# Optimization experiments

Hardware: AMD Instinct MI355X
Metric: run time of the kernel (lower is better)

## Reference

```python
import jax, jax.numpy as jnp
import numpy as np

STATE_DIM = 256
MAX_NODES = 64
EPS = 1e-5
EDGE_THRESHOLD = 0.3


def _glorot(key, shape):
    fan_in = shape[0]
    bound = 1.0 / np.sqrt(fan_in)
    return jax.random.uniform(key, shape, jnp.float32, -bound, bound)


def setup_inputs() -> dict:
    key = jax.random.key(0)
    ks = jax.random.split(key, 16)
    D = STATE_DIM
    d2, d4 = D // 2, D // 4
    inp = {
        "state_sequence": jax.random.normal(ks[0], (256, 128, D), jnp.float32),
        # node encoder
        "W1": _glorot(ks[1], (D, d2)), "b1": jnp.zeros((d2,), jnp.float32),
        "W2": _glorot(ks[2], (d2, d4)), "b2": jnp.zeros((d4,), jnp.float32),
        "gamma": jnp.ones((d4,), jnp.float32), "beta": jnp.zeros((d4,), jnp.float32),
        # edge predictor (input dim d2 = 2*d4)
        "E1": _glorot(ks[3], (d2, 64)), "bE1": jnp.zeros((64,), jnp.float32),
        "E2": _glorot(ks[4], (64, 32)), "bE2": jnp.zeros((32,), jnp.float32),
        "E3": _glorot(ks[5], (32, 1)), "bE3": jnp.zeros((1,), jnp.float32),
        # strength estimator
        "S1": _glorot(ks[6], (d2, 32)), "bS1": jnp.zeros((32,), jnp.float32),
        "S2": _glorot(ks[7], (32, 1)), "bS2": jnp.zeros((1,), jnp.float32),
    }
    return inp


def reference(state_sequence, W1, b1, W2, b2, gamma, beta,
              E1, bE1, E2, bE2, E3, bE3, S1, bS1, S2, bS2):
    B, S, D = state_sequence.shape
    N = MAX_NODES
    # pad if seq shorter than max_nodes (static shapes, here S >= N so no-op branch)
    if S < N:
        state_sequence = jnp.pad(state_sequence, ((0, 0), (0, N - S), (0, 0)))
        S = N
    # linspace indices, truncated to long like torch.linspace(..., dtype=long)
    idx = jnp.linspace(0.0, S - 1, N).astype(jnp.int32)
    nodes = state_sequence[:, idx]                      # [B, N, D]

    # node encoder: Linear -> ReLU -> (Dropout eval) -> Linear -> LayerNorm
    h = jax.nn.relu(jnp.einsum('bnd,de->bne', nodes, W1) + b1)
    h = jnp.einsum('bnd,de->bne', h, W2) + b2           # [B, N, D//4]
    mu = jnp.mean(h, axis=-1, keepdims=True)
    var = jnp.mean((h - mu) ** 2, axis=-1, keepdims=True)
    node_features = (h - mu) * jax.lax.rsqrt(var + EPS) * gamma + beta
    node_features = jnp.nan_to_num(node_features, nan=0.0)

    d4 = node_features.shape[-1]
    # pair input is concat([f_i, f_j]); split first-layer weights to avoid
    # materializing the [B,N,N,2*d4] concat tensor.
    # edge predictor first layer
    ei = jnp.einsum('bnd,dh->bnh', node_features, E1[:d4])   # [B, N, 64]
    ej = jnp.einsum('bnd,dh->bnh', node_features, E1[d4:])
    he = jax.nn.relu(ei[:, :, None, :] + ej[:, None, :, :] + bE1)  # [B,N,N,64]
    he = jax.nn.relu(jnp.einsum('bijh,hk->bijk', he, E2) + bE2)    # [B,N,N,32]
    edge_prob = jax.nn.sigmoid(jnp.einsum('bijk,ko->bijo', he, E3) + bE3)[..., 0]

    # strength estimator
    si = jnp.einsum('bnd,dh->bnh', node_features, S1[:d4])
    sj = jnp.einsum('bnd,dh->bnh', node_features, S1[d4:])
    hs = jax.nn.relu(si[:, :, None, :] + sj[:, None, :, :] + bS1)  # [B,N,N,32]
    strength = jnp.tanh(jnp.einsum('bijk,ko->bijo', hs, S2) + bS2)[..., 0]

    offdiag = 1.0 - jnp.eye(N, dtype=edge_prob.dtype)   # i != j only
    adjacency = edge_prob * offdiag
    strengths = strength * offdiag
    adjacency = jnp.where(adjacency > EDGE_THRESHOLD, adjacency, 0.0)
    return node_features, adjacency, strengths
```

## Files before the change

### kernel.cpp

```cpp
#include <hip/hip_runtime.h>
#include <hip/hip_bf16.h>
#include <math.h>

typedef __attribute__((ext_vector_type(8))) short short8;
typedef __attribute__((ext_vector_type(4))) short short4v;
typedef __attribute__((ext_vector_type(4))) float f32x4;
typedef __attribute__((ext_vector_type(2))) _Float16 h2;
typedef __attribute__((ext_vector_type(4))) _Float16 h4;
typedef __attribute__((ext_vector_type(8))) _Float16 h8;

__device__ __forceinline__ short f2bf(float f) {
    __hip_bfloat16 h = __float2bfloat16(f);
    return __builtin_bit_cast(short, h);
}

__global__ __launch_bounds__(256)
void kernelA0(const float* __restrict__ W1, const float* __restrict__ W2,
              const float* __restrict__ E1, const float* __restrict__ S1,
              short* __restrict__ wT)
{
    const int tid = blockIdx.x * 256 + threadIdx.x;
    {
        const int k = tid >> 7, n = tid & 127;
        wT[n * 256 + k] = f2bf(W1[tid]);
    }
    if (tid < 8192) {
        const int k = tid >> 6, n = tid & 63;
        wT[32768 + n * 128 + k] = f2bf(W2[tid]);
    }
    if (tid < 8192) {
        const int rr = tid >> 6, c = tid & 63;
        const int o = (rr < 64) ? c : (64 + c);
        const int k = (rr < 64) ? rr : (rr - 64);
        wT[40960 + o * 64 + k] = f2bf(E1[tid]);
    }
    if (tid < 4096) {
        const int rr = tid >> 5, c = tid & 31;
        const int o = (rr < 64) ? (128 + c) : (160 + c);
        const int k = (rr < 64) ? rr : (rr - 64);
        wT[40960 + o * 64 + k] = f2bf(S1[tid]);
    }
}

constexpr int XS_S  = 264;
constexpr int H1B_S = 136;
constexpr int HS_S  = 68;
constexpr int NNF_S = 72;
constexpr int EJW   = 72;
constexpr int SJW   = 40;

constexpr int OFF_XS  = 0;
constexpr int OFF_EIH = 0;
constexpr int OFF_EJH = 9216;
constexpr int OFF_SIH = 18432;
constexpr int OFF_SJH = 23552;
constexpr int OFF_H1B = 33792;
constexpr int OFF_HS  = 51200;
constexpr int LDS_BYTES = 68608;

__global__ __launch_bounds__(1024)
void kernelF(const float* __restrict__ x,
             const float* __restrict__ b1, const float* __restrict__ b2,
             const float* __restrict__ gamma, const float* __restrict__ beta,
             const short* __restrict__ wT,
             const float* __restrict__ bE1, const float* __restrict__ E2,
             const float* __restrict__ bE2, const float* __restrict__ E3,
             const float* __restrict__ bE3, const float* __restrict__ bS1,
             const float* __restrict__ S2, const float* __restrict__ bS2,
             float* __restrict__ out_nf, float* __restrict__ out_adj,
             float* __restrict__ out_str)
{
    extern __shared__ char lds[];
    short*    XsS  = (short*)(lds + OFF_XS);
    short*    h1BS = (short*)(lds + OFF_H1B);
    float*    HsS  = (float*)(lds + OFF_HS);
    short*    nfBS = (short*)(lds + OFF_H1B);
    _Float16* eihS = (_Float16*)(lds + OFF_EIH);
    _Float16* ejhS = (_Float16*)(lds + OFF_EJH);
    _Float16* sihS = (_Float16*)(lds + OFF_SIH);
    _Float16* sjhS = (_Float16*)(lds + OFF_SJH);
    __shared__ float bE2s[32], E3s[32];
    __shared__ _Float16 s2hS[32];

    const int t = threadIdx.x, b = blockIdx.x;
    const int w = t >> 6, l = t & 63, g = l >> 4, r = l & 15;
    const short* W1T = wT;
    const short* W2T = wT + 32768;
    const short* WcT = wT + 40960;

    if (t < 32)       bE2s[t] = bE2[t];
    else if (t < 64)  E3s[t - 32] = E3[t - 32];
    else if (t < 96)  s2hS[t - 64] = (_Float16)S2[t - 64];

    h8 aE00, aE10, aE01, aE11;
#pragma unroll
    for (int e = 0; e < 8; ++e) {
        aE00[e] = (_Float16)E2[(size_t)(8 * g + e) * 32 + r];
        aE10[e] = (_Float16)E2[(size_t)(8 * g + e + 32) * 32 + r];
        aE01[e] = (_Float16)E2[(size_t)(8 * g + e) * 32 + r + 16];
        aE11[e] = (_Float16)E2[(size_t)(8 * g + e + 32) * 32 + r + 16];
    }
    const float bE3v = bE3[0], bS2v = bS2[0];
    const h8 z8 = {(_Float16)0.f, (_Float16)0.f, (_Float16)0.f, (_Float16)0.f,
                   (_Float16)0.f, (_Float16)0.f, (_Float16)0.f, (_Float16)0.f};

    {
        const int row = t >> 4, c0 = t & 15;
        const int srow = (row == 63) ? 127 : (int)((float)row * (127.0f / 63.0f));
        const float* xrow = x + ((size_t)b * 128 + srow) * 256;
#pragma unroll
        for (int i = 0; i < 4; ++i) {
            const int c4 = (c0 + 16 * i) * 4;
            const float4 v = *(const float4*)(xrow + c4);
            short4v s;
            s[0] = f2bf(v.x); s[1] = f2bf(v.y); s[2] = f2bf(v.z); s[3] = f2bf(v.w);
            *(short4v*)&XsS[row * XS_S + c4] = s;
        }
    }
    __syncthreads();

    {
        const int mt = w >> 2, nb = (w & 3) << 1;
        const int aRow = (16 * mt + r) * XS_S;
#pragma unroll
        for (int np = 0; np < 2; ++np) {
            const int n = ((nb + np) << 4) + r;
            f32x4 acca = {0.f, 0.f, 0.f, 0.f};
            f32x4 accb = {0.f, 0.f, 0.f, 0.f};
#pragma unroll
            for (int ks = 0; ks < 4; ++ks) {
                const short8 a0  = *(const short8*)&XsS[aRow + 32 * ks + 8 * g];
                const short8 a1  = *(const short8*)&XsS[aRow + 32 * (ks + 4) + 8 * g];
                const short8 bwa = *(const short8*)(W1T + (size_t)n * 256 + 32 * ks + 8 * g);
                const short8 bwb = *(const short8*)(W1T + (size_t)n * 256 + 32 * (ks + 4) + 8 * g);
                acca = __builtin_amdgcn_mfma_f32_16x16x32_bf16(a0, bwa, acca, 0, 0, 0);
                accb = __builtin_amdgcn_mfma_f32_16x16x32_bf16(a1, bwb, accb, 0, 0, 0);
            }
            const float b1v = b1[n];
#pragma unroll
            for (int q = 0; q < 4; ++q)
                h1BS[(16 * mt + 4 * g + q) * H1B_S + n] = f2bf(fmaxf(acca[q] + accb[q] + b1v, 0.f));
        }
    }
    __syncthreads();

    {
        const int mt = w >> 2;
        const int n = ((w & 3) << 4) + r;
        const int aRow = (16 * mt + r) * H1B_S;
        f32x4 acca = {0.f, 0.f, 0.f, 0.f};
        f32x4 accb = {0.f, 0.f, 0.f, 0.f};
#pragma unroll
        for (int ks2 = 0; ks2 < 2; ++ks2) {
            const short8 ha0 = *(const short8*)&h1BS[aRow + 32 * (2 * ks2) + 8 * g];
            const short8 ha1 = *(const short8*)&h1BS[aRow + 32 * (2 * ks2 + 1) + 8 * g];
            const short8 bw0 = *(const short8*)(W2T + (size_t)n * 128 + 32 * (2 * ks2) + 8 * g);
            const short8 bw1 = *(const short8*)(W2T + (size_t)n * 128 + 32 * (2 * ks2 + 1) + 8 * g);
            acca = __builtin_amdgcn_mfma_f32_16x16x32_bf16(ha0, bw0, acca, 0, 0, 0);
            accb = __builtin_amdgcn_mfma_f32_16x16x32_bf16(ha1, bw1, accb, 0, 0, 0);
        }
        const float b2v = b2[n];
#pragma unroll
        for (int q = 0; q < 4; ++q)
            HsS[(16 * mt + 4 * g + q) * HS_S + n] = acca[q] + accb[q] + b2v;
    }
    __syncthreads();

    {
        const int row = t >> 4, c4 = (t & 15) * 4;
        const float4 v = *(const float4*)&HsS[row * HS_S + c4];
        float s = v.x + v.y + v.z + v.w;
        s += __shfl_xor(s, 1); s += __shfl_xor(s, 2);
        s += __shfl_xor(s, 4); s += __shfl_xor(s, 8);
        const float mu = s * (1.0f / 64.0f);
        float vs = 0.f;
        { const float d0 = v.x-mu, d1 = v.y-mu, d2 = v.z-mu, d3 = v.w-mu;
          vs = fmaf(d0,d0, fmaf(d1,d1, fmaf(d2,d2, d3*d3))); }
        vs += __shfl_xor(vs, 1); vs += __shfl_xor(vs, 2);
        vs += __shfl_xor(vs, 4); vs += __shfl_xor(vs, 8);
        const float rstd = rsqrtf(vs * (1.0f / 64.0f) + 1e-5f);
        const float4 gv = *(const float4*)(gamma + c4);
        const float4 bv = *(const float4*)(beta  + c4);
        float4 o;
        o.x = fmaf((v.x - mu) * rstd, gv.x, bv.x);
        o.y = fmaf((v.y - mu) * rstd, gv.y, bv.y);
        o.z = fmaf((v.z - mu) * rstd, gv.z, bv.z);
        o.w = fmaf((v.w - mu) * rstd, gv.w, bv.w);
        *(float4*)(out_nf + (size_t)b * 4096 + (size_t)row * 64 + c4) = o;
        short4v ob;
        ob[0] = f2bf(o.x); ob[1] = f2bf(o.y); ob[2] = f2bf(o.z); ob[3] = f2bf(o.w);
        *(short4v*)&nfBS[row * NNF_S + c4] = ob;
    }
    __syncthreads();

    {
        const int mt = w >> 2;
        const short8 na0 = *(const short8*)&nfBS[(16 * mt + r) * NNF_S + 8 * g];
        const short8 na1 = *(const short8*)&nfBS[(16 * mt + r) * NNF_S + 32 + 8 * g];
#pragma unroll
        for (int k3 = 0; k3 < 3; ++k3) {
            const int ot = (w & 3) * 3 + k3;
            const int c = 16 * ot + r;
            const short8 bw0 = *(const short8*)(WcT + (size_t)c * 64 + 8 * g);
            const short8 bw1 = *(const short8*)(WcT + (size_t)c * 64 + 32 + 8 * g);
            f32x4 acc = {0.f, 0.f, 0.f, 0.f};
            acc = __builtin_amdgcn_mfma_f32_16x16x32_bf16(na0, bw0, acc, 0, 0, 0);
            acc = __builtin_amdgcn_mfma_f32_16x16x32_bf16(na1, bw1, acc, 0, 0, 0);
            if (ot < 4) {
                const float bv = bE1[c];
#pragma unroll
                for (int q = 0; q < 4; ++q)
                    eihS[(16 * mt + 4 * g + q) * EJW + c] = (_Float16)(acc[q] + bv);
            } else if (ot < 8) {
#pragma unroll
                for (int q = 0; q < 4; ++q)
                    ejhS[(16 * mt + 4 * g + q) * EJW + (c - 64)] = (_Float16)acc[q];
            } else if (ot < 10) {
                const float bv = bS1[c - 128];
#pragma unroll
                for (int q = 0; q < 4; ++q)
                    sihS[(16 * mt + 4 * g + q) * SJW + (c - 128)] = (_Float16)(acc[q] + bv);
            } else {
#pragma unroll
                for (int q = 0; q < 4; ++q)
                    sjhS[(16 * mt + 4 * g + q) * SJW + (c - 160)] = (_Float16)acc[q];
            }
        }
    }
    __syncthreads();

    for (int jt = 0; jt < 4; ++jt) {
        const int j = (jt << 4) + r;
        const h8 ej0 = *(const h8*)&ejhS[j * EJW + 8 * g];
        const h8 ej1 = *(const h8*)&ejhS[j * EJW + 32 + 8 * g];

#pragma unroll
        for (int ii = 0; ii < 4; ++ii) {
            const int ig = 4 * w + ii;
            const h8 ei0 = *(const h8*)&eihS[ig * EJW + 8 * g];
            const h8 ei1 = *(const h8*)&eihS[ig * EJW + 32 + 8 * g];

            const h8 b0 = __builtin_elementwise_max(ei0 + ej0, z8);
            const h8 b1 = __builtin_elementwise_max(ei1 + ej1, z8);

            f32x4 acc0 = {0.f, 0.f, 0.f, 0.f};
            f32x4 acc1 = {0.f, 0.f, 0.f, 0.f};
            acc0 = __builtin_amdgcn_mfma_f32_16x16x32_f16(aE00, b0, acc0, 0, 0, 0);
            acc0 = __builtin_amdgcn_mfma_f32_16x16x32_f16(aE10, b1, acc0, 0, 0, 0);
            acc1 = __builtin_amdgcn_mfma_f32_16x16x32_f16(aE01, b0, acc1, 0, 0, 0);
            acc1 = __builtin_amdgcn_mfma_f32_16x16x32_f16(aE11, b1, acc1, 0, 0, 0);

            float pe = 0.f;
#pragma unroll
            for (int q = 0; q < 4; ++q) {
                const int k0 = 4 * g + q;
                pe = fmaf(fmaxf(acc0[q] + bE2s[k0], 0.f), E3s[k0], pe);
                pe = fmaf(fmaxf(acc1[q] + bE2s[k0 + 16], 0.f), E3s[k0 + 16], pe);
            }
            pe += __shfl_xor(pe, 16);
            pe += __shfl_xor(pe, 32);

            if (l < 16) {
                const float z = pe + bE3v;
                const float p = 1.0f / (1.0f + __expf(-z));
                const float av = (j == ig || !(p > 0.3f)) ? 0.f : p;
                out_adj[(size_t)b * 4096 + (size_t)ig * 64 + j] = av;
            }
        }
    }

    {
        const int j = t & 63;
        const int ib = (t >> 6) * 4;
#pragma unroll
        for (int ii = 0; ii < 4; ++ii) {
            const int ig = ib + ii;
            float sacc = 0.f;
#pragma unroll
            for (int c = 0; c < 4; ++c) {
                const h8 si8 = *(const h8*)&sihS[ig * SJW + 8 * c];
                const h8 sj8 = *(const h8*)&sjhS[j * SJW + 8 * c];
                const h8 s2  = *(const h8*)&s2hS[8 * c];
                const h8 hs = __builtin_elementwise_max(si8 + sj8, z8);
                const h2 p0 = __builtin_shufflevector(hs, hs, 0, 1);
                const h2 p1 = __builtin_shufflevector(hs, hs, 2, 3);
                const h2 p2 = __builtin_shufflevector(hs, hs, 4, 5);
                const h2 p3 = __builtin_shufflevector(hs, hs, 6, 7);
                const h2 q0 = __builtin_shufflevector(s2, s2, 0, 1);
                const h2 q1 = __builtin_shufflevector(s2, s2, 2, 3);
                const h2 q2 = __builtin_shufflevector(s2, s2, 4, 5);
                const h2 q3 = __builtin_shufflevector(s2, s2, 6, 7);
                sacc = __builtin_amdgcn_fdot2(p0, q0, sacc, false);
                sacc = __builtin_amdgcn_fdot2(p1, q1, sacc, false);
                sacc = __builtin_amdgcn_fdot2(p2, q2, sacc, false);
                sacc = __builtin_amdgcn_fdot2(p3, q3, sacc, false);
            }
            const float xs = sacc + bS2v;
            const float e2x = __expf(2.0f * xs);
            const float sv = (j == ig) ? 0.f : (e2x - 1.0f) / (e2x + 1.0f);
            out_str[(size_t)b * 4096 + (size_t)ig * 64 + j] = sv;
        }
    }
}

extern "C" void kernel_launch(void* const* d_in, const int* in_sizes, int n_in,
                              void* d_out, int out_size, void* d_ws, size_t ws_size,
                              hipStream_t stream)
{
    const float* x     = (const float*)d_in[0];
    const float* W1    = (const float*)d_in[1];
    const float* b1    = (const float*)d_in[2];
    const float* W2    = (const float*)d_in[3];
    const float* b2    = (const float*)d_in[4];
    const float* gamma = (const float*)d_in[5];
    const float* beta  = (const float*)d_in[6];
    const float* E1    = (const float*)d_in[7];
    const float* bE1   = (const float*)d_in[8];
    const float* E2    = (const float*)d_in[9];
    const float* bE2   = (const float*)d_in[10];
    const float* E3    = (const float*)d_in[11];
    const float* bE3   = (const float*)d_in[12];
    const float* S1    = (const float*)d_in[13];
    const float* bS1   = (const float*)d_in[14];
    const float* S2    = (const float*)d_in[15];
    const float* bS2   = (const float*)d_in[16];

    float* out     = (float*)d_out;
    float* out_nf  = out;
    float* out_adj = out + 1048576;
    float* out_str = out + 2097152;

    short* wT = (short*)d_ws;

    (void)hipFuncSetAttribute((const void*)kernelF,
        hipFuncAttributeMaxDynamicSharedMemorySize, LDS_BYTES);

    kernelA0<<<128, 256, 0, stream>>>(W1, W2, E1, S1, wT);

    kernelF<<<256, 1024, LDS_BYTES, stream>>>(
        x, b1, b2, gamma, beta, wT,
        bE1, E2, bE2, E3, bE3, bS1, S2, bS2,
        out_nf, out_adj, out_str);
}
```

Measured before the change: 38.45 us.

## Split each batch across two 512-thread blocks, duplicating node encoder work

Launches a 2x256 grid of 512-thread blocks instead of 256 blocks of 1024 threads. Each block recomputes the full node encoder and projections for its batch element, then handles half of the i-rows of the pairwise edge and strength stages. Only block s==0 writes node features. The aim is more blocks across the CUs and better occupancy, paid for by computing the encoder and projections twice per batch element.

```diff
diff --git a/kernel.cpp b/kernel.cpp
--- a/kernel.cpp
+++ b/kernel.cpp
@@ -6,7 +6,6 @@
 typedef __attribute__((ext_vector_type(4))) short short4v;
 typedef __attribute__((ext_vector_type(4))) float f32x4;
 typedef __attribute__((ext_vector_type(2))) _Float16 h2;
-typedef __attribute__((ext_vector_type(4))) _Float16 h4;
 typedef __attribute__((ext_vector_type(8))) _Float16 h8;
 
 __device__ __forceinline__ short f2bf(float f) {
@@ -58,7 +57,7 @@
 constexpr int OFF_HS  = 51200;
 constexpr int LDS_BYTES = 68608;
 
-__global__ __launch_bounds__(1024)
+__global__ __launch_bounds__(512)
 void kernelF(const float* __restrict__ x,
              const float* __restrict__ b1, const float* __restrict__ b2,
              const float* __restrict__ gamma, const float* __restrict__ beta,
@@ -82,7 +81,9 @@
     __shared__ float bE2s[32], E3s[32];
     __shared__ _Float16 s2hS[32];
 
-    const int t = threadIdx.x, b = blockIdx.x;
+    const int t = threadIdx.x;
+    const int s = blockIdx.x;
+    const int b = blockIdx.y;
     const int w = t >> 6, l = t & 63, g = l >> 4, r = l & 15;
     const short* W1T = wT;
     const short* W2T = wT + 32768;
@@ -105,25 +106,25 @@
                    (_Float16)0.f, (_Float16)0.f, (_Float16)0.f, (_Float16)0.f};
 
     {
-        const int row = t >> 4, c0 = t & 15;
+        const int row = t >> 3, c0 = t & 7;
         const int srow = (row == 63) ? 127 : (int)((float)row * (127.0f / 63.0f));
         const float* xrow = x + ((size_t)b * 128 + srow) * 256;
 #pragma unroll
-        for (int i = 0; i < 4; ++i) {
-            const int c4 = (c0 + 16 * i) * 4;
+        for (int i = 0; i < 8; ++i) {
+            const int c4 = (c0 + 8 * i) * 4;
             const float4 v = *(const float4*)(xrow + c4);
-            short4v s;
-            s[0] = f2bf(v.x); s[1] = f2bf(v.y); s[2] = f2bf(v.z); s[3] = f2bf(v.w);
-            *(short4v*)&XsS[row * XS_S + c4] = s;
-        }
-    }
-    __syncthreads();
-
-    {
-        const int mt = w >> 2, nb = (w & 3) << 1;
+            short4v sv4;
+            sv4[0] = f2bf(v.x); sv4[1] = f2bf(v.y); sv4[2] = f2bf(v.z); sv4[3] = f2bf(v.w);
+            *(short4v*)&XsS[row * XS_S + c4] = sv4;
+        }
+    }
+    __syncthreads();
+
+    {
+        const int mt = w >> 1, nb = (w & 1) << 2;
         const int aRow = (16 * mt + r) * XS_S;
 #pragma unroll
-        for (int np = 0; np < 2; ++np) {
+        for (int np = 0; np < 4; ++np) {
             const int n = ((nb + np) << 4) + r;
             f32x4 acca = {0.f, 0.f, 0.f, 0.f};
             f32x4 accb = {0.f, 0.f, 0.f, 0.f};
@@ -145,34 +146,38 @@
     __syncthreads();
 
     {
-        const int mt = w >> 2;
-        const int n = ((w & 3) << 4) + r;
+        const int mt = w >> 1;
         const int aRow = (16 * mt + r) * H1B_S;
-        f32x4 acca = {0.f, 0.f, 0.f, 0.f};
-        f32x4 accb = {0.f, 0.f, 0.f, 0.f};
-#pragma unroll
-        for (int ks2 = 0; ks2 < 2; ++ks2) {
-            const short8 ha0 = *(const short8*)&h1BS[aRow + 32 * (2 * ks2) + 8 * g];
-            const short8 ha1 = *(const short8*)&h1BS[aRow + 32 * (2 * ks2 + 1) + 8 * g];
-            const short8 bw0 = *(const short8*)(W2T + (size_t)n * 128 + 32 * (2 * ks2) + 8 * g);
-            const short8 bw1 = *(const short8*)(W2T + (size_t)n * 128 + 32 * (2 * ks2 + 1) + 8 * g);
-            acca = __builtin_amdgcn_mfma_f32_16x16x32_bf16(ha0, bw0, acca, 0, 0, 0);
-            accb = __builtin_amdgcn_mfma_f32_16x16x32_bf16(ha1, bw1, accb, 0, 0, 0);
-        }
-        const float b2v = b2[n];
-#pragma unroll
-        for (int q = 0; q < 4; ++q)
-            HsS[(16 * mt + 4 * g + q) * HS_S + n] = acca[q] + accb[q] + b2v;
-    }
-    __syncthreads();
-
-    {
-        const int row = t >> 4, c4 = (t & 15) * 4;
+#pragma unroll
+        for (int p = 0; p < 2; ++p) {
+            const int n = (((w & 1) * 2 + p) << 4) + r;
+            f32x4 acca = {0.f, 0.f, 0.f, 0.f};
+            f32x4 accb = {0.f, 0.f, 0.f, 0.f};
+#pragma unroll
+            for (int ks2 = 0; ks2 < 2; ++ks2) {
+                const short8 ha0 = *(const short8*)&h1BS[aRow + 32 * (2 * ks2) + 8 * g];
+                const short8 ha1 = *(const short8*)&h1BS[aRow + 32 * (2 * ks2 + 1) + 8 * g];
+                const short8 bw0 = *(const short8*)(W2T + (size_t)n * 128 + 32 * (2 * ks2) + 8 * g);
+                const short8 bw1 = *(const short8*)(W2T + (size_t)n * 128 + 32 * (2 * ks2 + 1) + 8 * g);
+                acca = __builtin_amdgcn_mfma_f32_16x16x32_bf16(ha0, bw0, acca, 0, 0, 0);
+                accb = __builtin_amdgcn_mfma_f32_16x16x32_bf16(ha1, bw1, accb, 0, 0, 0);
+            }
+            const float b2v = b2[n];
+#pragma unroll
+            for (int q = 0; q < 4; ++q)
+                HsS[(16 * mt + 4 * g + q) * HS_S + n] = acca[q] + accb[q] + b2v;
+        }
+    }
+    __syncthreads();
+
+#pragma unroll
+    for (int it = 0; it < 2; ++it) {
+        const int row = (t >> 4) + 32 * it, c4 = (t & 15) * 4;
         const float4 v = *(const float4*)&HsS[row * HS_S + c4];
-        float s = v.x + v.y + v.z + v.w;
-        s += __shfl_xor(s, 1); s += __shfl_xor(s, 2);
-        s += __shfl_xor(s, 4); s += __shfl_xor(s, 8);
-        const float mu = s * (1.0f / 64.0f);
+        float sm = v.x + v.y + v.z + v.w;
+        sm += __shfl_xor(sm, 1); sm += __shfl_xor(sm, 2);
+        sm += __shfl_xor(sm, 4); sm += __shfl_xor(sm, 8);
+        const float mu = sm * (1.0f / 64.0f);
         float vs = 0.f;
         { const float d0 = v.x-mu, d1 = v.y-mu, d2 = v.z-mu, d3 = v.w-mu;
           vs = fmaf(d0,d0, fmaf(d1,d1, fmaf(d2,d2, d3*d3))); }
@@ -186,7 +191,8 @@
         o.y = fmaf((v.y - mu) * rstd, gv.y, bv.y);
         o.z = fmaf((v.z - mu) * rstd, gv.z, bv.z);
         o.w = fmaf((v.w - mu) * rstd, gv.w, bv.w);
-        *(float4*)(out_nf + (size_t)b * 4096 + (size_t)row * 64 + c4) = o;
+        if (s == 0)
+            *(float4*)(out_nf + (size_t)b * 4096 + (size_t)row * 64 + c4) = o;
         short4v ob;
         ob[0] = f2bf(o.x); ob[1] = f2bf(o.y); ob[2] = f2bf(o.z); ob[3] = f2bf(o.w);
         *(short4v*)&nfBS[row * NNF_S + c4] = ob;
@@ -194,12 +200,12 @@
     __syncthreads();
 
     {
-        const int mt = w >> 2;
+        const int mt = w >> 1;
         const short8 na0 = *(const short8*)&nfBS[(16 * mt + r) * NNF_S + 8 * g];
         const short8 na1 = *(const short8*)&nfBS[(16 * mt + r) * NNF_S + 32 + 8 * g];
 #pragma unroll
-        for (int k3 = 0; k3 < 3; ++k3) {
-            const int ot = (w & 3) * 3 + k3;
+        for (int k6 = 0; k6 < 6; ++k6) {
+            const int ot = (w & 1) * 6 + k6;
             const int c = 16 * ot + r;
             const short8 bw0 = *(const short8*)(WcT + (size_t)c * 64 + 8 * g);
             const short8 bw1 = *(const short8*)(WcT + (size_t)c * 64 + 32 + 8 * g);
@@ -236,7 +242,7 @@
 
 #pragma unroll
         for (int ii = 0; ii < 4; ++ii) {
-            const int ig = 4 * w + ii;
+            const int ig = 32 * s + 4 * w + ii;
             const h8 ei0 = *(const h8*)&eihS[ig * EJW + 8 * g];
             const h8 ei1 = *(const h8*)&eihS[ig * EJW + 32 + 8 * g];
 
@@ -271,7 +277,7 @@
 
     {
         const int j = t & 63;
-        const int ib = (t >> 6) * 4;
+        const int ib = 32 * s + (t >> 6) * 4;
 #pragma unroll
         for (int ii = 0; ii < 4; ++ii) {
             const int ig = ib + ii;
@@ -337,7 +343,7 @@
 
     kernelA0<<<128, 256, 0, stream>>>(W1, W2, E1, S1, wT);
 
-    kernelF<<<256, 1024, LDS_BYTES, stream>>>(
+    kernelF<<<dim3(2, 256), 512, LDS_BYTES, stream>>>(
         x, b1, b2, gamma, beta, wT,
         bE1, E2, bE2, E3, bE3, bS1, S2, bS2,
         out_nf, out_adj, out_str);
```

Measured after the change: 47.74 us. 1.24x slower.

## Split fused kernel into node encoder and pairwise edge kernel with finer grid

Applied to the files above, without the earlier changes.

Splits the single per-batch fused kernel into a node-encoder kernel that writes per-node edge and strength projections to global workspace, and a separate pairwise kernel launched on an 8x256 grid of 256-thread blocks. Each pairwise block loads the j-side projections plus 8 i-rows into LDS and computes edge probabilities and strengths for that slice. This is meant to raise parallelism and occupancy in the pairwise phase, which previously ran as only 256 large blocks. In exchange it adds a kernel launch and a global round trip for the intermediate projections.

```diff
diff --git a/kernel.cpp b/kernel.cpp
--- a/kernel.cpp
+++ b/kernel.cpp
@@ -6,7 +6,6 @@
 typedef __attribute__((ext_vector_type(4))) short short4v;
 typedef __attribute__((ext_vector_type(4))) float f32x4;
 typedef __attribute__((ext_vector_type(2))) _Float16 h2;
-typedef __attribute__((ext_vector_type(4))) _Float16 h4;
 typedef __attribute__((ext_vector_type(8))) _Float16 h8;
 
 __device__ __forceinline__ short f2bf(float f) {
@@ -20,90 +19,54 @@
               short* __restrict__ wT)
 {
     const int tid = blockIdx.x * 256 + threadIdx.x;
-    {
-        const int k = tid >> 7, n = tid & 127;
-        wT[n * 256 + k] = f2bf(W1[tid]);
-    }
+    {   const int k = tid >> 7, n = tid & 127;
+        wT[n * 256 + k] = f2bf(W1[tid]); }
     if (tid < 8192) {
         const int k = tid >> 6, n = tid & 63;
-        wT[32768 + n * 128 + k] = f2bf(W2[tid]);
-    }
+        wT[32768 + n * 128 + k] = f2bf(W2[tid]); }
     if (tid < 8192) {
         const int rr = tid >> 6, c = tid & 63;
         const int o = (rr < 64) ? c : (64 + c);
         const int k = (rr < 64) ? rr : (rr - 64);
-        wT[40960 + o * 64 + k] = f2bf(E1[tid]);
-    }
+        wT[40960 + o * 64 + k] = f2bf(E1[tid]); }
     if (tid < 4096) {
         const int rr = tid >> 5, c = tid & 31;
         const int o = (rr < 64) ? (128 + c) : (160 + c);
         const int k = (rr < 64) ? rr : (rr - 64);
-        wT[40960 + o * 64 + k] = f2bf(S1[tid]);
-    }
+        wT[40960 + o * 64 + k] = f2bf(S1[tid]); }
 }
 
 constexpr int XS_S  = 264;
 constexpr int H1B_S = 136;
 constexpr int HS_S  = 68;
 constexpr int NNF_S = 72;
-constexpr int EJW   = 72;
-constexpr int SJW   = 40;
-
 constexpr int OFF_XS  = 0;
-constexpr int OFF_EIH = 0;
-constexpr int OFF_EJH = 9216;
-constexpr int OFF_SIH = 18432;
-constexpr int OFF_SJH = 23552;
 constexpr int OFF_H1B = 33792;
 constexpr int OFF_HS  = 51200;
-constexpr int LDS_BYTES = 68608;
+constexpr int LDS_BYTES_N = 68608;
 
 __global__ __launch_bounds__(1024)
-void kernelF(const float* __restrict__ x,
+void kernelN(const float* __restrict__ x,
              const float* __restrict__ b1, const float* __restrict__ b2,
              const float* __restrict__ gamma, const float* __restrict__ beta,
              const short* __restrict__ wT,
-             const float* __restrict__ bE1, const float* __restrict__ E2,
-             const float* __restrict__ bE2, const float* __restrict__ E3,
-             const float* __restrict__ bE3, const float* __restrict__ bS1,
-             const float* __restrict__ S2, const float* __restrict__ bS2,
-             float* __restrict__ out_nf, float* __restrict__ out_adj,
-             float* __restrict__ out_str)
+             const float* __restrict__ bE1, const float* __restrict__ bS1,
+             float* __restrict__ out_nf,
+             _Float16* __restrict__ wei, _Float16* __restrict__ wej,
+             _Float16* __restrict__ wsi, _Float16* __restrict__ wsj)
 {
     extern __shared__ char lds[];
-    short*    XsS  = (short*)(lds + OFF_XS);
-    short*    h1BS = (short*)(lds + OFF_H1B);
-    float*    HsS  = (float*)(lds + OFF_HS);
-    short*    nfBS = (short*)(lds + OFF_H1B);
-    _Float16* eihS = (_Float16*)(lds + OFF_EIH);
-    _Float16* ejhS = (_Float16*)(lds + OFF_EJH);
-    _Float16* sihS = (_Float16*)(lds + OFF_SIH);
-    _Float16* sjhS = (_Float16*)(lds + OFF_SJH);
-    __shared__ float bE2s[32], E3s[32];
-    __shared__ _Float16 s2hS[32];
+    short* XsS  = (short*)(lds + OFF_XS);
+    short* h1BS = (short*)(lds + OFF_H1B);
+    float* HsS  = (float*)(lds + OFF_HS);
+    short* nfBS = (short*)(lds + OFF_H1B);
 
     const int t = threadIdx.x, b = blockIdx.x;
-    const int w = t >> 6, l = t & 63, g = l >> 4, r = l & 15;
+    const int w = t >> 6, g = (t & 63) >> 4, r = t & 15;
     const short* W1T = wT;
     const short* W2T = wT + 32768;
     const short* WcT = wT + 40960;
 
-    if (t < 32)       bE2s[t] = bE2[t];
-    else if (t < 64)  E3s[t - 32] = E3[t - 32];
-    else if (t < 96)  s2hS[t - 64] = (_Float16)S2[t - 64];
-
-    h8 aE00, aE10, aE01, aE11;
-#pragma unroll
-    for (int e = 0; e < 8; ++e) {
-        aE00[e] = (_Float16)E2[(size_t)(8 * g + e) * 32 + r];
-        aE10[e] = (_Float16)E2[(size_t)(8 * g + e + 32) * 32 + r];
-        aE01[e] = (_Float16)E2[(size_t)(8 * g + e) * 32 + r + 16];
-        aE11[e] = (_Float16)E2[(size_t)(8 * g + e + 32) * 32 + r + 16];
-    }
-    const float bE3v = bE3[0], bS2v = bS2[0];
-    const h8 z8 = {(_Float16)0.f, (_Float16)0.f, (_Float16)0.f, (_Float16)0.f,
-                   (_Float16)0.f, (_Float16)0.f, (_Float16)0.f, (_Float16)0.f};
-
     {
         const int row = t >> 4, c0 = t & 15;
         const int srow = (row == 63) ? 127 : (int)((float)row * (127.0f / 63.0f));
@@ -112,9 +75,9 @@
         for (int i = 0; i < 4; ++i) {
             const int c4 = (c0 + 16 * i) * 4;
             const float4 v = *(const float4*)(xrow + c4);
-            short4v s;
-            s[0] = f2bf(v.x); s[1] = f2bf(v.y); s[2] = f2bf(v.z); s[3] = f2bf(v.w);
-            *(short4v*)&XsS[row * XS_S + c4] = s;
+            short4v sv;
+            sv[0] = f2bf(v.x); sv[1] = f2bf(v.y); sv[2] = f2bf(v.z); sv[3] = f2bf(v.w);
+            *(short4v*)&XsS[row * XS_S + c4] = sv;
         }
     }
     __syncthreads();
@@ -210,35 +173,94 @@
                 const float bv = bE1[c];
 #pragma unroll
                 for (int q = 0; q < 4; ++q)
-                    eihS[(16 * mt + 4 * g + q) * EJW + c] = (_Float16)(acc[q] + bv);
+                    wei[(size_t)b * 4096 + (size_t)(16 * mt + 4 * g + q) * 64 + c] = (_Float16)(acc[q] + bv);
             } else if (ot < 8) {
 #pragma unroll
                 for (int q = 0; q < 4; ++q)
-                    ejhS[(16 * mt + 4 * g + q) * EJW + (c - 64)] = (_Float16)acc[q];
+                    wej[(size_t)b * 4096 + (size_t)(16 * mt + 4 * g + q) * 64 + (c - 64)] = (_Float16)acc[q];
             } else if (ot < 10) {
                 const float bv = bS1[c - 128];
 #pragma unroll
                 for (int q = 0; q < 4; ++q)
-                    sihS[(16 * mt + 4 * g + q) * SJW + (c - 128)] = (_Float16)(acc[q] + bv);
+                    wsi[(size_t)b * 2048 + (size_t)(16 * mt + 4 * g + q) * 32 + (c - 128)] = (_Float16)(acc[q] + bv);
             } else {
 #pragma unroll
                 for (int q = 0; q < 4; ++q)
-                    sjhS[(16 * mt + 4 * g + q) * SJW + (c - 160)] = (_Float16)acc[q];
-            }
-        }
-    }
+                    wsj[(size_t)b * 2048 + (size_t)(16 * mt + 4 * g + q) * 32 + (c - 160)] = (_Float16)acc[q];
+            }
+        }
+    }
+}
+
+constexpr int BEJ = 72;
+constexpr int BSJ = 40;
+
+__global__ __launch_bounds__(256, 4)
+void kernelB(const _Float16* __restrict__ wei, const _Float16* __restrict__ wej,
+             const _Float16* __restrict__ wsi, const _Float16* __restrict__ wsj,
+             const float* __restrict__ E2,
+             const float* __restrict__ bE2, const float* __restrict__ E3,
+             const float* __restrict__ bE3,
+             const float* __restrict__ S2, const float* __restrict__ bS2,
+             float* __restrict__ out_adj, float* __restrict__ out_str)
+{
+    __shared__ _Float16 ejH[64 * BEJ];
+    __shared__ _Float16 eiH[8 * BEJ];
+    __shared__ _Float16 sjH[64 * BSJ];
+    __shared__ _Float16 siH[8 * BSJ];
+    __shared__ float bE2s[32], E3s[32];
+    __shared__ _Float16 s2hS[32];
+
+    const int t = threadIdx.x;
+    const int s = blockIdx.x;
+    const int b = blockIdx.y;
+    const int w = t >> 6, l = t & 63, g = l >> 4, r = l & 15;
+
+#pragma unroll
+    for (int it = 0; it < 2; ++it) {
+        const int c = t + 256 * it; const int row = c >> 3, k8 = c & 7;
+        *(h8*)&ejH[row * BEJ + 8 * k8] = *(const h8*)&wej[(size_t)b * 4096 + row * 64 + 8 * k8];
+    }
+    if (t < 64) {
+        const int row = t >> 3, k8 = t & 7;
+        *(h8*)&eiH[row * BEJ + 8 * k8] = *(const h8*)&wei[(size_t)b * 4096 + (size_t)(8 * s + row) * 64 + 8 * k8];
+    }
+    {
+        const int row = t >> 2, k8 = t & 3;
+        *(h8*)&sjH[row * BSJ + 8 * k8] = *(const h8*)&wsj[(size_t)b * 2048 + row * 32 + 8 * k8];
+    }
+    if (t < 32) {
+        const int row = t >> 2, k8 = t & 3;
+        *(h8*)&siH[row * BSJ + 8 * k8] = *(const h8*)&wsi[(size_t)b * 2048 + (size_t)(8 * s + row) * 32 + 8 * k8];
+    }
+    if (t < 32)       bE2s[t] = bE2[t];
+    else if (t < 64)  E3s[t - 32] = E3[t - 32];
+    else if (t < 96)  s2hS[t - 64] = (_Float16)S2[t - 64];
+
+    h8 aE00, aE10, aE01, aE11;
+#pragma unroll
+    for (int e = 0; e < 8; ++e) {
+        aE00[e] = (_Float16)E2[(size_t)(8 * g + e) * 32 + r];
+        aE10[e] = (_Float16)E2[(size_t)(8 * g + e + 32) * 32 + r];
+        aE01[e] = (_Float16)E2[(size_t)(8 * g + e) * 32 + r + 16];
+        aE11[e] = (_Float16)E2[(size_t)(8 * g + e + 32) * 32 + r + 16];
+    }
+    const float bE3v = bE3[0], bS2v = bS2[0];
+    const h8 z8 = {(_Float16)0.f, (_Float16)0.f, (_Float16)0.f, (_Float16)0.f,
+                   (_Float16)0.f, (_Float16)0.f, (_Float16)0.f, (_Float16)0.f};
     __syncthreads();
 
     for (int jt = 0; jt < 4; ++jt) {
         const int j = (jt << 4) + r;
-        const h8 ej0 = *(const h8*)&ejhS[j * EJW + 8 * g];
-        const h8 ej1 = *(const h8*)&ejhS[j * EJW + 32 + 8 * g];
-
-#pragma unroll
-        for (int ii = 0; ii < 4; ++ii) {
-            const int ig = 4 * w + ii;
-            const h8 ei0 = *(const h8*)&eihS[ig * EJW + 8 * g];
-            const h8 ei1 = *(const h8*)&eihS[ig * EJW + 32 + 8 * g];
+        const h8 ej0 = *(const h8*)&ejH[j * BEJ + 8 * g];
+        const h8 ej1 = *(const h8*)&ejH[j * BEJ + 32 + 8 * g];
+
+#pragma unroll
+        for (int ii = 0; ii < 2; ++ii) {
+            const int il = 2 * w + ii;
+            const int ig = 8 * s + il;
+            const h8 ei0 = *(const h8*)&eiH[il * BEJ + 8 * g];
+            const h8 ei1 = *(const h8*)&eiH[il * BEJ + 32 + 8 * g];
 
             const h8 b0 = __builtin_elementwise_max(ei0 + ej0, z8);
             const h8 b1 = __builtin_elementwise_max(ei1 + ej1, z8);
@@ -271,15 +293,16 @@
 
     {
         const int j = t & 63;
-        const int ib = (t >> 6) * 4;
-#pragma unroll
-        for (int ii = 0; ii < 4; ++ii) {
-            const int ig = ib + ii;
+        const int lb = (t >> 6) * 2;
+#pragma unroll
+        for (int ii = 0; ii < 2; ++ii) {
+            const int il = lb + ii;
+            const int ig = 8 * s + il;
             float sacc = 0.f;
 #pragma unroll
             for (int c = 0; c < 4; ++c) {
-                const h8 si8 = *(const h8*)&sihS[ig * SJW + 8 * c];
-                const h8 sj8 = *(const h8*)&sjhS[j * SJW + 8 * c];
+                const h8 si8 = *(const h8*)&siH[il * BSJ + 8 * c];
+                const h8 sj8 = *(const h8*)&sjH[j * BSJ + 8 * c];
                 const h8 s2  = *(const h8*)&s2hS[8 * c];
                 const h8 hs = __builtin_elementwise_max(si8 + sj8, z8);
                 const h2 p0 = __builtin_shufflevector(hs, hs, 0, 1);
@@ -331,14 +354,23 @@
     float* out_str = out + 2097152;
 
     short* wT = (short*)d_ws;
-
-    (void)hipFuncSetAttribute((const void*)kernelF,
-        hipFuncAttributeMaxDynamicSharedMemorySize, LDS_BYTES);
+    _Float16* wsH = (_Float16*)d_ws;
+    _Float16* wei = wsH + 65536;
+    _Float16* wej = wei + 1048576;
+    _Float16* wsi = wej + 1048576;
+    _Float16* wsj = wsi + 524288;
+
+    (void)hipFuncSetAttribute((const void*)kernelN,
+        hipFuncAttributeMaxDynamicSharedMemorySize, LDS_BYTES_N);
 
     kernelA0<<<128, 256, 0, stream>>>(W1, W2, E1, S1, wT);
 
-    kernelF<<<256, 1024, LDS_BYTES, stream>>>(
-        x, b1, b2, gamma, beta, wT,
-        bE1, E2, bE2, E3, bE3, bS1, S2, bS2,
-        out_nf, out_adj, out_str);
-}
+    kernelN<<<256, 1024, LDS_BYTES_N, stream>>>(
+        x, b1, b2, gamma, beta, wT, bE1, bS1,
+        out_nf, wei, wej, wsi, wsj);
+
+    kernelB<<<dim3(8, 256), 256, 0, stream>>>(
+        wei, wej, wsi, wsj,
+        E2, bE2, E3, bE3, S2, bS2,
+        out_adj, out_str);
+}
```

Result: slower. 47.07 us (+22.4%).

## Use 32x32x16 MFMA for edge MLP with swizzled ej LDS layout

Applied to the files above, without the earlier changes.

Replaces the four 16x16x32 MFMAs per (i, 16-j tile) in the edge-predictor second layer with a chain of four 32x32x16 f16 MFMAs covering 32 j columns and all 32 outputs. ej rows in LDS are written with an XOR swizzle to avoid bank conflicts on the new access pattern. The bE2/E3 constants are permuted to match the 32x32 accumulator layout and read as vectors. This removes one cross-lane shuffle per reduction and halves the outer j loop, at the cost of a larger 16-register accumulator and more index arithmetic.

```diff
diff --git a/kernel.cpp b/kernel.cpp
--- a/kernel.cpp
+++ b/kernel.cpp
@@ -5,8 +5,8 @@
 typedef __attribute__((ext_vector_type(8))) short short8;
 typedef __attribute__((ext_vector_type(4))) short short4v;
 typedef __attribute__((ext_vector_type(4))) float f32x4;
+typedef __attribute__((ext_vector_type(16))) float f32x16;
 typedef __attribute__((ext_vector_type(2))) _Float16 h2;
-typedef __attribute__((ext_vector_type(4))) _Float16 h4;
 typedef __attribute__((ext_vector_type(8))) _Float16 h8;
 
 __device__ __forceinline__ short f2bf(float f) {
@@ -20,26 +20,21 @@
               short* __restrict__ wT)
 {
     const int tid = blockIdx.x * 256 + threadIdx.x;
-    {
-        const int k = tid >> 7, n = tid & 127;
-        wT[n * 256 + k] = f2bf(W1[tid]);
-    }
+    {   const int k = tid >> 7, n = tid & 127;
+        wT[n * 256 + k] = f2bf(W1[tid]); }
     if (tid < 8192) {
         const int k = tid >> 6, n = tid & 63;
-        wT[32768 + n * 128 + k] = f2bf(W2[tid]);
-    }
+        wT[32768 + n * 128 + k] = f2bf(W2[tid]); }
     if (tid < 8192) {
         const int rr = tid >> 6, c = tid & 63;
         const int o = (rr < 64) ? c : (64 + c);
         const int k = (rr < 64) ? rr : (rr - 64);
-        wT[40960 + o * 64 + k] = f2bf(E1[tid]);
-    }
+        wT[40960 + o * 64 + k] = f2bf(E1[tid]); }
     if (tid < 4096) {
         const int rr = tid >> 5, c = tid & 31;
         const int o = (rr < 64) ? (128 + c) : (160 + c);
         const int k = (rr < 64) ? rr : (rr - 64);
-        wT[40960 + o * 64 + k] = f2bf(S1[tid]);
-    }
+        wT[40960 + o * 64 + k] = f2bf(S1[tid]); }
 }
 
 constexpr int XS_S  = 264;
@@ -79,27 +74,34 @@
     _Float16* ejhS = (_Float16*)(lds + OFF_EJH);
     _Float16* sihS = (_Float16*)(lds + OFF_SIH);
     _Float16* sjhS = (_Float16*)(lds + OFF_SJH);
-    __shared__ float bE2s[32], E3s[32];
+    __shared__ float bE2p[32], E3p[32];
     __shared__ _Float16 s2hS[32];
 
     const int t = threadIdx.x, b = blockIdx.x;
     const int w = t >> 6, l = t & 63, g = l >> 4, r = l & 15;
+    const int ehi = l >> 5, ec = l & 31;
     const short* W1T = wT;
     const short* W2T = wT + 32768;
     const short* WcT = wT + 40960;
 
-    if (t < 32)       bE2s[t] = bE2[t];
-    else if (t < 64)  E3s[t - 32] = E3[t - 32];
-    else if (t < 96)  s2hS[t - 64] = (_Float16)S2[t - 64];
-
-    h8 aE00, aE10, aE01, aE11;
-#pragma unroll
-    for (int e = 0; e < 8; ++e) {
-        aE00[e] = (_Float16)E2[(size_t)(8 * g + e) * 32 + r];
-        aE10[e] = (_Float16)E2[(size_t)(8 * g + e + 32) * 32 + r];
-        aE01[e] = (_Float16)E2[(size_t)(8 * g + e) * 32 + r + 16];
-        aE11[e] = (_Float16)E2[(size_t)(8 * g + e + 32) * 32 + r + 16];
-    }
+    if (t < 32) {
+        const int row = t;
+        const int pos = ((row >> 2) & 1) * 16 + (row >> 3) * 4 + (row & 3);
+        bE2p[pos] = bE2[row];
+    } else if (t < 64) {
+        const int row = t - 32;
+        const int pos = ((row >> 2) & 1) * 16 + (row >> 3) * 4 + (row & 3);
+        E3p[pos] = E3[row];
+    } else if (t < 96) {
+        s2hS[t - 64] = (_Float16)S2[t - 64];
+    }
+
+    h8 aE[4];
+#pragma unroll
+    for (int ks = 0; ks < 4; ++ks)
+#pragma unroll
+        for (int e = 0; e < 8; ++e)
+            aE[ks][e] = (_Float16)E2[(size_t)(16 * ks + 8 * ehi + e) * 32 + ec];
     const float bE3v = bE3[0], bS2v = bS2[0];
     const h8 z8 = {(_Float16)0.f, (_Float16)0.f, (_Float16)0.f, (_Float16)0.f,
                    (_Float16)0.f, (_Float16)0.f, (_Float16)0.f, (_Float16)0.f};
@@ -112,9 +114,9 @@
         for (int i = 0; i < 4; ++i) {
             const int c4 = (c0 + 16 * i) * 4;
             const float4 v = *(const float4*)(xrow + c4);
-            short4v s;
-            s[0] = f2bf(v.x); s[1] = f2bf(v.y); s[2] = f2bf(v.z); s[3] = f2bf(v.w);
-            *(short4v*)&XsS[row * XS_S + c4] = s;
+            short4v sv;
+            sv[0] = f2bf(v.x); sv[1] = f2bf(v.y); sv[2] = f2bf(v.z); sv[3] = f2bf(v.w);
+            *(short4v*)&XsS[row * XS_S + c4] = sv;
         }
     }
     __syncthreads();
@@ -212,9 +214,12 @@
                 for (int q = 0; q < 4; ++q)
                     eihS[(16 * mt + 4 * g + q) * EJW + c] = (_Float16)(acc[q] + bv);
             } else if (ot < 8) {
-#pragma unroll
-                for (int q = 0; q < 4; ++q)
-                    ejhS[(16 * mt + 4 * g + q) * EJW + (c - 64)] = (_Float16)acc[q];
+                const int cc = c - 64, ci = cc >> 3, lo = cc & 7;
+#pragma unroll
+                for (int q = 0; q < 4; ++q) {
+                    const int row = 16 * mt + 4 * g + q;
+                    ejhS[row * EJW + ((ci ^ ((row >> 3) & 3)) << 3) + lo] = (_Float16)acc[q];
+                }
             } else if (ot < 10) {
                 const float bv = bS1[c - 128];
 #pragma unroll
@@ -229,38 +234,33 @@
     }
     __syncthreads();
 
-    for (int jt = 0; jt < 4; ++jt) {
-        const int j = (jt << 4) + r;
-        const h8 ej0 = *(const h8*)&ejhS[j * EJW + 8 * g];
-        const h8 ej1 = *(const h8*)&ejhS[j * EJW + 32 + 8 * g];
-
+    for (int jt = 0; jt < 2; ++jt) {
+        const int j = 32 * jt + ec;
+        const int swz = (j >> 3) & 3;
 #pragma unroll
         for (int ii = 0; ii < 4; ++ii) {
             const int ig = 4 * w + ii;
-            const h8 ei0 = *(const h8*)&eihS[ig * EJW + 8 * g];
-            const h8 ei1 = *(const h8*)&eihS[ig * EJW + 32 + 8 * g];
-
-            const h8 b0 = __builtin_elementwise_max(ei0 + ej0, z8);
-            const h8 b1 = __builtin_elementwise_max(ei1 + ej1, z8);
-
-            f32x4 acc0 = {0.f, 0.f, 0.f, 0.f};
-            f32x4 acc1 = {0.f, 0.f, 0.f, 0.f};
-            acc0 = __builtin_amdgcn_mfma_f32_16x16x32_f16(aE00, b0, acc0, 0, 0, 0);
-            acc0 = __builtin_amdgcn_mfma_f32_16x16x32_f16(aE10, b1, acc0, 0, 0, 0);
-            acc1 = __builtin_amdgcn_mfma_f32_16x16x32_f16(aE01, b0, acc1, 0, 0, 0);
-            acc1 = __builtin_amdgcn_mfma_f32_16x16x32_f16(aE11, b1, acc1, 0, 0, 0);
-
+            f32x16 acc = {0.f,0.f,0.f,0.f, 0.f,0.f,0.f,0.f,
+                          0.f,0.f,0.f,0.f, 0.f,0.f,0.f,0.f};
+#pragma unroll
+            for (int ks = 0; ks < 4; ++ks) {
+                const int ci = 2 * ks + ehi;
+                const h8 ej = *(const h8*)&ejhS[j * EJW + ((ci ^ swz) << 3)];
+                const h8 ei = *(const h8*)&eihS[ig * EJW + 16 * ks + 8 * ehi];
+                const h8 bb = __builtin_elementwise_max(ei + ej, z8);
+                acc = __builtin_amdgcn_mfma_f32_32x32x16_f16(aE[ks], bb, acc, 0, 0, 0);
+            }
             float pe = 0.f;
 #pragma unroll
-            for (int q = 0; q < 4; ++q) {
-                const int k0 = 4 * g + q;
-                pe = fmaf(fmaxf(acc0[q] + bE2s[k0], 0.f), E3s[k0], pe);
-                pe = fmaf(fmaxf(acc1[q] + bE2s[k0 + 16], 0.f), E3s[k0 + 16], pe);
-            }
-            pe += __shfl_xor(pe, 16);
+            for (int p = 0; p < 4; ++p) {
+                const f32x4 bb2 = *(const f32x4*)&bE2p[ehi * 16 + 4 * p];
+                const f32x4 e3  = *(const f32x4*)&E3p[ehi * 16 + 4 * p];
+#pragma unroll
+                for (int q = 0; q < 4; ++q)
+                    pe = fmaf(fmaxf(acc[4 * p + q] + bb2[q], 0.f), e3[q], pe);
+            }
             pe += __shfl_xor(pe, 32);
-
-            if (l < 16) {
+            if (l < 32) {
                 const float z = pe + bE3v;
                 const float p = 1.0f / (1.0f + __expf(-z));
                 const float av = (j == ig || !(p > 0.3f)) ? 0.f : p;
```

Result: slower. 55.97 us (+45.6%).
